# Performance work log

Hardware: AMD Instinct MI355X
Metric: run time of the kernel (lower is better)

The kernel has to match this reference:

```python
import jax, jax.numpy as jnp
import numpy as np
from jax import lax

K = 3       # kernel_size
STRIDE = 1
PAD = 1
DIL = 1


def setup_inputs() -> dict:
    key = jax.random.key(0)
    ks = jax.random.split(key, 4)
    B, Cin, Cout, H, W = 4, 128, 256, 64, 64
    x = jax.random.normal(ks[0], (B, Cin, H, W), jnp.float32)
    # offset/mask conv params: out channels = 3*K*K (groups=1). Small weights
    # keep predicted offsets within a few pixels (module inits them to zero).
    om_w = jax.random.normal(ks[1], (3 * K * K, Cin, K, K), jnp.float32) * 0.01
    om_b = jnp.zeros((3 * K * K,), jnp.float32)
    weight = jax.random.normal(ks[2], (Cout, Cin, K, K), jnp.float32) * (1.0 / np.sqrt(Cin * K * K))
    bias = jnp.zeros((Cout,), jnp.float32)
    return {"x": x, "om_w": om_w, "om_b": om_b, "weight": weight, "bias": bias}


def _deform_conv(x, om_w, om_b, weight, bias):
    B, Cin, H, W = x.shape
    Cout = weight.shape[0]
    kk = K * K

    # offset/mask conv (stride/pad/dilation same as main conv)
    om = lax.conv_general_dilated(
        x, om_w, (STRIDE, STRIDE), [(PAD, PAD), (PAD, PAD)],
        rhs_dilation=(DIL, DIL), dimension_numbers=('NCHW', 'OIHW', 'NCHW'))
    om = om + om_b[None, :, None, None]
    Ho, Wo = om.shape[2], om.shape[3]

    off = om[:, :2 * kk].reshape(B, 2, kk, Ho, Wo)
    off_x, off_y = off[:, 0], off[:, 1]           # [B,kk,Ho,Wo]
    mask = jax.nn.sigmoid(om[:, 2 * kk:])          # [B,kk,Ho,Wo]

    # base grid (output pixel -> input pixel of kernel center)
    gy, gx = jnp.meshgrid(jnp.arange(Ho, dtype=x.dtype), jnp.arange(Wo, dtype=x.dtype), indexing='ij')
    base_x = gx * STRIDE - PAD
    base_y = gy * STRIDE - PAD
    # kernel taps centered at 0: arange(-(K-1)//2, (K+1)//2)
    r = jnp.arange(-(K - 1) // 2, (K + 1) // 2, dtype=x.dtype)
    koy, kox = jnp.meshgrid(r * DIL, r * DIL, indexing='ij')
    kox = kox.reshape(kk, 1, 1)
    koy = koy.reshape(kk, 1, 1)

    sx = base_x[None, None] + kox[None] + off_x    # [B,kk,Ho,Wo]
    sy = base_y[None, None] + koy[None] + off_y

    # Faithful to original: coords normalized with align_corners=True formula
    # (2*s/(size-1)-1) but grid_sample called with align_corners=False, i.e.
    # pixel coord = ((g+1)*size - 1)/2  =>  s*size/(size-1) - 0.5
    ix = sx * (W / (W - 1.0)) - 0.5
    iy = sy * (H / (H - 1.0)) - 0.5

    x0 = jnp.floor(ix)
    y0 = jnp.floor(iy)
    x1 = x0 + 1.0
    y1 = y0 + 1.0
    wx1 = ix - x0
    wx0 = 1.0 - wx1
    wy1 = iy - y0
    wy0 = 1.0 - wy1

    img = x.reshape(B, Cin, H * W)

    def gather(yy, xx):
        yi = yy.astype(jnp.int32)
        xi = xx.astype(jnp.int32)
        valid = ((yi >= 0) & (yi < H) & (xi >= 0) & (xi < W)).astype(x.dtype)
        idx = jnp.clip(yi, 0, H - 1) * W + jnp.clip(xi, 0, W - 1)   # [B,kk,Ho,Wo]
        v = jax.vmap(lambda im, i: im[:, i])(img, idx.reshape(B, -1))  # [B,Cin,kk*Ho*Wo]
        return v.reshape(B, Cin, kk, Ho, Wo) * valid[:, None]

    # bilinear (zeros padding) sample at kk taps per output pixel
    sampled = (gather(y0, x0) * (wy0 * wx0)[:, None]
               + gather(y0, x1) * (wy0 * wx1)[:, None]
               + gather(y1, x0) * (wy1 * wx0)[:, None]
               + gather(y1, x1) * (wy1 * wx1)[:, None])   # [B,Cin,kk,Ho,Wo]

    sampled = sampled * mask[:, None]
    w = weight.reshape(Cout, Cin, kk)
    out = jnp.einsum('bckhw,ock->bohw', sampled, w)
    return out + bias[None, :, None, None]


def reference(x, om_w, om_b, weight, bias):
    return _deform_conv(x, om_w, om_b, weight, bias)
```

## Files before the change

kernel.cpp:

```cpp
#include <hip/hip_runtime.h>
#include <hip/hip_bf16.h>

typedef _Float16 h4 __attribute__((ext_vector_type(4)));
typedef _Float16 h8 __attribute__((ext_vector_type(8)));
typedef float f32x4 __attribute__((ext_vector_type(4)));

#define CIN 128
#define COUT 256
#define KDIM (CIN*9)

__global__ __launch_bounds__(256) void k_pt(const float* __restrict__ x,
                                            const float* __restrict__ wgt,
                                            const float* __restrict__ om_w,
                                            unsigned short* __restrict__ xT,
                                            unsigned short* __restrict__ Wf,
                                            unsigned short* __restrict__ omWf) {
    __shared__ unsigned short tile[64][132];
    const int bid = blockIdx.x;
    if (bid < 256) {
        const int b = bid >> 6, y = bid & 63;
        const float* xp = x + (size_t)b * CIN * 4096 + y * 64;
        const int w = threadIdx.x & 63, cg = threadIdx.x >> 6;
#pragma unroll
        for (int cc = 0; cc < CIN; cc += 4) {
            int c = cc + cg;
            _Float16 hv = (_Float16)xp[(size_t)c * 4096 + w];
            tile[w][c] = *(unsigned short*)&hv;
        }
        __syncthreads();
        unsigned short* orow = xT + (size_t)(b * 4096 + y * 64) * CIN;
#pragma unroll
        for (int i = 0; i < 8; ++i) {
            int j = threadIdx.x + i * 256;
            int w2 = j >> 5, c2 = (j & 31) * 4;
            ushort4 v = *(ushort4*)&tile[w2][c2];
            ((ushort4*)orow)[j] = v;
        }
    } else if (bid < 1408) {
        int g = (bid - 256) * 256 + threadIdx.x;
        int o = g / KDIM, rem = g - o * KDIM;
        int c = rem / 9, k = rem - c * 9;
        int kc = k * 128 + c;
        int kch = kc >> 5, j = kc & 31;
        int l = ((j >> 3) << 4) | (o & 15);
        int e = j & 7, of = o >> 4;
        int f = ((kch * 16 + of) * 64 + l) * 8 + e;
        _Float16 hv = (_Float16)wgt[g];
        Wf[f] = *(unsigned short*)&hv;
    } else {
        int f = (bid - 1408) * 256 + threadIdx.x;
        int e = f & 7, l = (f >> 3) & 63, of = (f >> 9) & 1, kch = f >> 10;
        int o = of * 16 + (l & 15);
        int c = (kch & 3) * 32 + (l >> 4) * 8 + e;
        int k = kch >> 2;
        float v = (o < 27) ? om_w[(size_t)o * KDIM + c * 9 + k] : 0.f;
        _Float16 hv = (_Float16)v;
        omWf[f] = *(unsigned short*)&hv;
    }
}

__global__ __launch_bounds__(512, 2) void k_fused(const unsigned short* __restrict__ xT_u,
                                                  const unsigned short* __restrict__ omWf_u,
                                                  const float* __restrict__ om_b,
                                                  const unsigned short* __restrict__ Wf_u,
                                                  const float* __restrict__ bias,
                                                  float* __restrict__ out) {
    const int bid = blockIdx.x;
    const int half = bid & 1, h = (bid >> 1) & 63, b = bid >> 7;
    const int p_base = half * 32;
    const int tid = threadIdx.x;
    const int wv = tid >> 6, lane = tid & 63;
    const int khalf = lane >> 4, lr = lane & 15;

    __shared__ int   s_off[4][288];
    __shared__ float s_wt[4][288];
    __shared__ h8    s_tile[2][32 * 16];
    __shared__ float red[4][32][28];

    const _Float16* xb = (const _Float16*)xT_u + (size_t)b * (4096 * CIN);

    {
        const h8* Af = (const h8*)omWf_u;
        const int pg = wv & 1, tg = wv >> 1;
        const int pl = pg * 16 + lr;
        const int p = p_base + pl;
        const int k0 = (tg == 0) ? 0 : 2 * tg + 1;
        const int k1 = (tg == 0) ? 3 : k0 + 2;
        f32x4 acc0 = (f32x4){0.f, 0.f, 0.f, 0.f};
        f32x4 acc1 = (f32x4){0.f, 0.f, 0.f, 0.f};
        for (int k = k0; k < k1; ++k) {
            const int ky = k / 3, kx = k - ky * 3;
            const int y = h + ky - 1, xq = p + kx - 1;
            const bool valid = ((unsigned)y < 64u) && ((unsigned)xq < 64u);
            const _Float16* src = xb + ((y * 64 + xq) * CIN);
#pragma unroll
            for (int cg = 0; cg < 4; ++cg) {
                h8 bf = {};
                if (valid) bf = *(const h8*)(src + cg * 32 + khalf * 8);
                const int kch = k * 4 + cg;
                h8 a0 = Af[(kch * 2 + 0) * 64 + lane];
                h8 a1 = Af[(kch * 2 + 1) * 64 + lane];
                acc0 = __builtin_amdgcn_mfma_f32_16x16x32_f16(a0, bf, acc0, 0, 0, 0);
                acc1 = __builtin_amdgcn_mfma_f32_16x16x32_f16(a1, bf, acc1, 0, 0, 0);
            }
        }
#pragma unroll
        for (int r = 0; r < 4; ++r) {
            red[tg][pl][khalf * 4 + r] = acc0[r];
            int row1 = 16 + khalf * 4 + r;
            if (row1 < 27) red[tg][pl][row1] = acc1[r];
        }
    }
    __syncthreads();

    for (int e = tid; e < 288; e += 512) {
        int k = e >> 5, pl = e & 31;
        int p = p_base + pl;
        float offx = red[0][pl][k]      + red[1][pl][k]      + red[2][pl][k]      + red[3][pl][k]      + om_b[k];
        float offy = red[0][pl][9 + k]  + red[1][pl][9 + k]  + red[2][pl][9 + k]  + red[3][pl][9 + k]  + om_b[9 + k];
        float mv   = red[0][pl][18 + k] + red[1][pl][18 + k] + red[2][pl][18 + k] + red[3][pl][18 + k] + om_b[18 + k];
        float mask = 1.f / (1.f + __expf(-mv));
        int ky = k / 3, kx = k - ky * 3;
        const float SC = 64.f / 63.f;
        float ix = ((float)(p + kx - 2) + offx) * SC - 0.5f;
        float iy = ((float)(h + ky - 2) + offy) * SC - 0.5f;
        float fx0 = floorf(ix), fy0 = floorf(iy);
        float wx1 = ix - fx0, wx0 = 1.f - wx1;
        float wy1 = iy - fy0, wy0 = 1.f - wy1;
        int x0 = (int)fx0, y0 = (int)fy0;
        int x1 = x0 + 1, y1 = y0 + 1;
        bool vx0 = (unsigned)x0 < 64u, vx1 = (unsigned)x1 < 64u;
        bool vy0 = (unsigned)y0 < 64u, vy1 = (unsigned)y1 < 64u;
        int xc0 = min(max(x0, 0), 63), xc1 = min(max(x1, 0), 63);
        int yc0 = min(max(y0, 0), 63), yc1 = min(max(y1, 0), 63);
        s_off[0][e] = (yc0 * 64 + xc0) * CIN;
        s_off[1][e] = (yc0 * 64 + xc1) * CIN;
        s_off[2][e] = (yc1 * 64 + xc0) * CIN;
        s_off[3][e] = (yc1 * 64 + xc1) * CIN;
        s_wt[0][e] = (vy0 && vx0) ? wy0 * wx0 * mask : 0.f;
        s_wt[1][e] = (vy0 && vx1) ? wy0 * wx1 * mask : 0.f;
        s_wt[2][e] = (vy1 && vx0) ? wy1 * wx0 * mask : 0.f;
        s_wt[3][e] = (vy1 && vx1) ? wy1 * wx1 * mask : 0.f;
    }
    __syncthreads();

    const int p  = tid >> 4;
    const int ci = tid & 15;
    const h8* Wf8 = (const h8*)Wf_u;
    const int wslot = ci ^ (p & 7);

    f32x4 acc[2][2];
#pragma unroll
    for (int i = 0; i < 2; ++i)
#pragma unroll
        for (int j = 0; j < 2; ++j) acc[i][j] = (f32x4){0.f, 0.f, 0.f, 0.f};

    {
        const int e0 = p;
        const int cb = ci * 8;
        h8 v0 = *(const h8*)(xb + s_off[0][e0] + cb);
        h8 v1 = *(const h8*)(xb + s_off[1][e0] + cb);
        h8 v2 = *(const h8*)(xb + s_off[2][e0] + cb);
        h8 v3 = *(const h8*)(xb + s_off[3][e0] + cb);
        const float m0 = s_wt[0][e0], m1 = s_wt[1][e0], m2 = s_wt[2][e0], m3 = s_wt[3][e0];
        h8 pk;
#pragma unroll
        for (int j = 0; j < 8; ++j) {
            float r = m0 * (float)v0[j] + m1 * (float)v1[j]
                    + m2 * (float)v2[j] + m3 * (float)v3[j];
            pk[j] = (_Float16)r;
        }
        s_tile[0][p * 16 + wslot] = pk;
    }
    __syncthreads();

    for (int tap = 0; tap < 9; ++tap) {
        const int cur = tap & 1;
        const int nxt = tap + 1;

        h8 v0, v1, v2, v3;
        float m0, m1, m2, m3;
        if (nxt < 9) {
            const int e = nxt * 32 + p;
            const int cb = ci * 8;
            v0 = *(const h8*)(xb + s_off[0][e] + cb);
            v1 = *(const h8*)(xb + s_off[1][e] + cb);
            v2 = *(const h8*)(xb + s_off[2][e] + cb);
            v3 = *(const h8*)(xb + s_off[3][e] + cb);
            m0 = s_wt[0][e]; m1 = s_wt[1][e]; m2 = s_wt[2][e]; m3 = s_wt[3][e];
        }

#pragma unroll
        for (int ks = 0; ks < 4; ++ks) {
            const int kch = tap * 4 + ks;
            h8 a0 = Wf8[(kch * 16 + wv * 2 + 0) * 64 + lane];
            h8 a1 = Wf8[(kch * 16 + wv * 2 + 1) * 64 + lane];
#pragma unroll
            for (int pf = 0; pf < 2; ++pf) {
                const int row = pf * 16 + lr;
                const int slot = (ks * 4 + khalf) ^ (row & 7);
                h8 bf = s_tile[cur][row * 16 + slot];
                acc[0][pf] = __builtin_amdgcn_mfma_f32_16x16x32_f16(a0, bf, acc[0][pf], 0, 0, 0);
                acc[1][pf] = __builtin_amdgcn_mfma_f32_16x16x32_f16(a1, bf, acc[1][pf], 0, 0, 0);
            }
        }

        if (nxt < 9) {
            h8 pk;
#pragma unroll
            for (int j = 0; j < 8; ++j) {
                float r = m0 * (float)v0[j] + m1 * (float)v1[j]
                        + m2 * (float)v2[j] + m3 * (float)v3[j];
                pk[j] = (_Float16)r;
            }
            s_tile[cur ^ 1][p * 16 + wslot] = pk;
        }
        __syncthreads();
    }

    float* outb = out + (size_t)b * COUT * 4096 + h * 64 + p_base;
#pragma unroll
    for (int i = 0; i < 2; ++i) {
#pragma unroll
        for (int r = 0; r < 4; ++r) {
            const int o = wv * 32 + i * 16 + khalf * 4 + r;
            const float bo = bias[o];
            float* orow = outb + (size_t)o * 4096;
#pragma unroll
            for (int pf = 0; pf < 2; ++pf)
                orow[pf * 16 + lr] = acc[i][pf][r] + bo;
        }
    }
}

extern "C" void kernel_launch(void* const* d_in, const int* in_sizes, int n_in,
                              void* d_out, int out_size, void* d_ws, size_t ws_size,
                              hipStream_t stream) {
    const float* x    = (const float*)d_in[0];
    const float* om_w = (const float*)d_in[1];
    const float* om_b = (const float*)d_in[2];
    const float* wgt  = (const float*)d_in[3];
    const float* bias = (const float*)d_in[4];
    float* out = (float*)d_out;

    char* ws = (char*)d_ws;
    unsigned short* xT   = (unsigned short*)ws;
    unsigned short* Wf   = (unsigned short*)(ws + 4194304);
    unsigned short* omWf = (unsigned short*)(ws + 4194304 + 589824);

    k_pt   <<<1552, 256, 0, stream>>>(x, wgt, om_w, xT, Wf, omWf);
    k_fused<<<512, 512, 0, stream>>>(xT, omWf, om_b, Wf, bias, out);
}
```

Measured before the change: 41.17 us.

## Process a full 64-pixel output row per block with 1024 threads

Each block now covers a whole output row (64 pixels) instead of half a row, using 16 waves that each own 16 output channels across 4 pixel fragments, in place of 8 waves owning 32 channels across 2 fragments. The offset-conv stage is redistributed over the larger block, and the grid shrinks to 256 blocks. This halves the number of blocks and avoids the duplicated offset-conv halo work between row halves. In exchange there are fewer blocks to spread across CUs (256 on a large GPU), 1024-thread barriers, and more shared memory per block, which may reduce occupancy.

```diff
diff --git a/kernel.cpp b/kernel.cpp
--- a/kernel.cpp
+++ b/kernel.cpp
@@ -59,38 +59,36 @@
     }
 }
 
-__global__ __launch_bounds__(512, 2) void k_fused(const unsigned short* __restrict__ xT_u,
-                                                  const unsigned short* __restrict__ omWf_u,
-                                                  const float* __restrict__ om_b,
-                                                  const unsigned short* __restrict__ Wf_u,
-                                                  const float* __restrict__ bias,
-                                                  float* __restrict__ out) {
+__global__ __launch_bounds__(1024, 4) void k_fused(const unsigned short* __restrict__ xT_u,
+                                                   const unsigned short* __restrict__ omWf_u,
+                                                   const float* __restrict__ om_b,
+                                                   const unsigned short* __restrict__ Wf_u,
+                                                   const float* __restrict__ bias,
+                                                   float* __restrict__ out) {
     const int bid = blockIdx.x;
-    const int half = bid & 1, h = (bid >> 1) & 63, b = bid >> 7;
-    const int p_base = half * 32;
+    const int h = bid & 63, b = bid >> 6;
     const int tid = threadIdx.x;
     const int wv = tid >> 6, lane = tid & 63;
     const int khalf = lane >> 4, lr = lane & 15;
 
-    __shared__ int   s_off[4][288];
-    __shared__ float s_wt[4][288];
-    __shared__ h8    s_tile[2][32 * 16];
-    __shared__ float red[4][32][28];
+    __shared__ int   s_off[4][576];
+    __shared__ float s_wt[4][576];
+    __shared__ h8    s_tile[2][64 * 16];
+    __shared__ float red[4][64][28];
 
     const _Float16* xb = (const _Float16*)xT_u + (size_t)b * (4096 * CIN);
 
     {
         const h8* Af = (const h8*)omWf_u;
-        const int pg = wv & 1, tg = wv >> 1;
+        const int pg = wv & 3, tg = wv >> 2;
         const int pl = pg * 16 + lr;
-        const int p = p_base + pl;
         const int k0 = (tg == 0) ? 0 : 2 * tg + 1;
         const int k1 = (tg == 0) ? 3 : k0 + 2;
         f32x4 acc0 = (f32x4){0.f, 0.f, 0.f, 0.f};
         f32x4 acc1 = (f32x4){0.f, 0.f, 0.f, 0.f};
         for (int k = k0; k < k1; ++k) {
             const int ky = k / 3, kx = k - ky * 3;
-            const int y = h + ky - 1, xq = p + kx - 1;
+            const int y = h + ky - 1, xq = pl + kx - 1;
             const bool valid = ((unsigned)y < 64u) && ((unsigned)xq < 64u);
             const _Float16* src = xb + ((y * 64 + xq) * CIN);
 #pragma unroll
@@ -113,12 +111,11 @@
     }
     __syncthreads();
 
-    for (int e = tid; e < 288; e += 512) {
-        int k = e >> 5, pl = e & 31;
-        int p = p_base + pl;
-        float offx = red[0][pl][k]      + red[1][pl][k]      + red[2][pl][k]      + red[3][pl][k]      + om_b[k];
-        float offy = red[0][pl][9 + k]  + red[1][pl][9 + k]  + red[2][pl][9 + k]  + red[3][pl][9 + k]  + om_b[9 + k];
-        float mv   = red[0][pl][18 + k] + red[1][pl][18 + k] + red[2][pl][18 + k] + red[3][pl][18 + k] + om_b[18 + k];
+    for (int e = tid; e < 576; e += 1024) {
+        int k = e >> 6, p = e & 63;
+        float offx = red[0][p][k]      + red[1][p][k]      + red[2][p][k]      + red[3][p][k]      + om_b[k];
+        float offy = red[0][p][9 + k]  + red[1][p][9 + k]  + red[2][p][9 + k]  + red[3][p][9 + k]  + om_b[9 + k];
+        float mv   = red[0][p][18 + k] + red[1][p][18 + k] + red[2][p][18 + k] + red[3][p][18 + k] + om_b[18 + k];
         float mask = 1.f / (1.f + __expf(-mv));
         int ky = k / 3, kx = k - ky * 3;
         const float SC = 64.f / 63.f;
@@ -149,11 +146,9 @@
     const h8* Wf8 = (const h8*)Wf_u;
     const int wslot = ci ^ (p & 7);
 
-    f32x4 acc[2][2];
-#pragma unroll
-    for (int i = 0; i < 2; ++i)
-#pragma unroll
-        for (int j = 0; j < 2; ++j) acc[i][j] = (f32x4){0.f, 0.f, 0.f, 0.f};
+    f32x4 acc[4];
+#pragma unroll
+    for (int j = 0; j < 4; ++j) acc[j] = (f32x4){0.f, 0.f, 0.f, 0.f};
 
     {
         const int e0 = p;
@@ -181,7 +176,7 @@
         h8 v0, v1, v2, v3;
         float m0, m1, m2, m3;
         if (nxt < 9) {
-            const int e = nxt * 32 + p;
+            const int e = nxt * 64 + p;
             const int cb = ci * 8;
             v0 = *(const h8*)(xb + s_off[0][e] + cb);
             v1 = *(const h8*)(xb + s_off[1][e] + cb);
@@ -193,15 +188,13 @@
 #pragma unroll
         for (int ks = 0; ks < 4; ++ks) {
             const int kch = tap * 4 + ks;
-            h8 a0 = Wf8[(kch * 16 + wv * 2 + 0) * 64 + lane];
-            h8 a1 = Wf8[(kch * 16 + wv * 2 + 1) * 64 + lane];
-#pragma unroll
-            for (int pf = 0; pf < 2; ++pf) {
+            h8 a0 = Wf8[(kch * 16 + wv) * 64 + lane];
+#pragma unroll
+            for (int pf = 0; pf < 4; ++pf) {
                 const int row = pf * 16 + lr;
                 const int slot = (ks * 4 + khalf) ^ (row & 7);
                 h8 bf = s_tile[cur][row * 16 + slot];
-                acc[0][pf] = __builtin_amdgcn_mfma_f32_16x16x32_f16(a0, bf, acc[0][pf], 0, 0, 0);
-                acc[1][pf] = __builtin_amdgcn_mfma_f32_16x16x32_f16(a1, bf, acc[1][pf], 0, 0, 0);
+                acc[pf] = __builtin_amdgcn_mfma_f32_16x16x32_f16(a0, bf, acc[pf], 0, 0, 0);
             }
         }
 
@@ -218,18 +211,15 @@
         __syncthreads();
     }
 
-    float* outb = out + (size_t)b * COUT * 4096 + h * 64 + p_base;
-#pragma unroll
-    for (int i = 0; i < 2; ++i) {
-#pragma unroll
-        for (int r = 0; r < 4; ++r) {
-            const int o = wv * 32 + i * 16 + khalf * 4 + r;
-            const float bo = bias[o];
-            float* orow = outb + (size_t)o * 4096;
-#pragma unroll
-            for (int pf = 0; pf < 2; ++pf)
-                orow[pf * 16 + lr] = acc[i][pf][r] + bo;
-        }
+    float* outb = out + (size_t)b * COUT * 4096 + h * 64;
+#pragma unroll
+    for (int r = 0; r < 4; ++r) {
+        const int o = wv * 16 + khalf * 4 + r;
+        const float bo = bias[o];
+        float* orow = outb + (size_t)o * 4096;
+#pragma unroll
+        for (int pf = 0; pf < 4; ++pf)
+            orow[pf * 16 + lr] = acc[pf][r] + bo;
     }
 }
 
@@ -249,5 +239,5 @@
     unsigned short* omWf = (unsigned short*)(ws + 4194304 + 589824);
 
     k_pt   <<<1552, 256, 0, stream>>>(x, wgt, om_w, xT, Wf, omWf);
-    k_fused<<<512, 512, 0, stream>>>(xT, omWf, om_b, Wf, bias, out);
+    k_fused<<<256, 1024, 0, stream>>>(xT, omWf, om_b, Wf, bias, out);
 }
```

Result: faster. 40.17 us, median of 3 (-2.4%).
